# Performance work log

Measured on AMD Instinct MI355X. Metric: run time of the kernel, lower is better.

Reference implementation:

```python
import jax, jax.numpy as jnp
import numpy as np

KS = 3   # window kernel size
NH = 4   # num heads

def unfold3d(x, ks):
    # x: (B,C,D,H,W) -> (B,C,D*H*W, ks**3); matches torch unfold(2).unfold(3).unfold(4) ordering
    B, C, D, H, W = x.shape
    p = ks // 2
    xp = jnp.pad(x, ((0,0),(0,0),(p,p),(p,p),(p,p)))
    wins = [xp[:, :, i:i+D, j:j+H, k:k+W]
            for i in range(ks) for j in range(ks) for k in range(ks)]
    u = jnp.stack(wins, axis=-1)  # (B,C,D,H,W,ks^3)
    return u.reshape(B, C, D*H*W, ks**3)

def make_mask(D, H, W, ks):
    ones = jnp.ones((1, 1, D, H, W), jnp.float32)
    return unfold3d(ones, ks)[0, 0] == 0  # (N, ks^3), True = out-of-bounds (masked)

def l2norm(x, eps=1e-12):
    n = jnp.sqrt(jnp.sum(x * x, axis=-1, keepdims=True))
    return x / jnp.maximum(n, eps)

def layernorm(x, g, b, eps=1e-5):
    m = x.mean(-1, keepdims=True)
    v = x.var(-1, keepdims=True)
    return (x - m) / jnp.sqrt(v + eps) * g + b

def conv3d(x, w, b, pad):
    y = jax.lax.conv_general_dilated(x, w, (1,1,1), [(pad,pad)]*3,
        dimension_numbers=('NCDHW', 'OIDHW', 'NCDHW'))
    return y + b.reshape(1, -1, 1, 1, 1)

def bnorm(x, g, b, eps=1e-5):
    # BatchNorm3d, training-mode batch statistics (biased variance)
    m = x.mean(axis=(0,2,3,4), keepdims=True)
    v = ((x - m) ** 2).mean(axis=(0,2,3,4), keepdims=True)
    return (x - m) / jnp.sqrt(v + eps) * g.reshape(1,-1,1,1,1) + b.reshape(1,-1,1,1,1)

def lrelu(x):
    return jnp.where(x > 0, x, 0.01 * x)

def resblock(x, w1, b1, g1, be1, w2, b2, g2, be2):
    # monai UnetResBlock, in==out, stride 1 -> identity residual
    y = lrelu(bnorm(conv3d(x, w1, b1, 1), g1, be1))
    y = bnorm(conv3d(y, w2, b2, 1), g2, be2)
    return lrelu(y + x)

def epa(x, D, H, W, mask, qkvv_w, temp, temp2, rpb, qemb, op1_w, op1_b, op2_w, op2_b):
    B, N, C = x.shape
    hd = C // NH
    qkvv = (x @ qkvv_w.T).reshape(B, N, 4, NH, hd).transpose(2, 0, 3, 1, 4)  # (4,B,NH,N,hd)
    q, k, v_ca, v_sa = qkvv[0], qkvv[1], qkvv[2], qkvv[3]
    # ---- spatial (local window) attention ----
    qns = (l2norm(q) + qemb) * jax.nn.softplus(temp2)  # (B,NH,N,hd)
    k_flat = k.transpose(0, 1, 3, 2).reshape(B, C, N)
    v_flat = v_sa.transpose(0, 1, 3, 2).reshape(B, C, N)
    k_loc = unfold3d(k_flat.reshape(B, C, D, H, W), KS).reshape(B, NH, hd, N, KS**3).transpose(0, 1, 3, 2, 4)
    v_loc = unfold3d(v_flat.reshape(B, C, D, H, W), KS).reshape(B, NH, hd, N, KS**3).transpose(0, 1, 3, 2, 4)
    attn_sa = jnp.einsum('bhnd,bhndk->bhnk', qns, k_loc) + rpb[None, :, None, :]
    attn_sa = jnp.where(mask[None, None], -jnp.inf, attn_sa)
    attn_sa = jax.nn.softmax(attn_sa, axis=-1)
    # NOTE: original torch code reshapes (B,NH,N,hd) directly to (B,N,C); replicate exactly
    x_sa = jnp.einsum('bhnk,bhndk->bhnd', attn_sa, v_loc).reshape(B, N, C)
    # ---- channel (cosine) cross-attention ----
    qt = l2norm(q.transpose(0, 1, 3, 2))  # (B,NH,hd,N), normalized over N
    kt = l2norm(k.transpose(0, 1, 3, 2))
    attn_ca = jax.nn.softmax(jnp.einsum('bhdn,bhen->bhde', qt, kt) * temp, axis=-1)
    x_ca = jnp.einsum('bhde,bhen->bhdn', attn_ca, v_ca.transpose(0, 1, 3, 2)).transpose(0, 3, 1, 2).reshape(B, N, C)
    return jnp.concatenate([x_sa @ op1_w.T + op1_b, x_ca @ op2_w.T + op2_b], axis=-1)


def setup_inputs() -> dict:
    key = jax.random.key(0)
    B, C, H, W, D = 1, 64, 32, 32, 32
    hd = C // NH
    ks = iter(jax.random.split(key, 40))
    def nrm(shape, s=0.02):
        return jax.random.normal(next(ks), shape, jnp.float32) * s
    inp = {
        'x': jax.random.normal(next(ks), (B, C, H, W, D), jnp.float32),
        'ln_g': jnp.ones((C,), jnp.float32), 'ln_b': jnp.zeros((C,), jnp.float32),
        'gamma': 1e-6 * jnp.ones((C,), jnp.float32),
        'qkvv_w': nrm((4 * C, C)),
        'temp': jnp.ones((NH, 1, 1), jnp.float32), 'temp2': jnp.ones((NH, 1, 1), jnp.float32),
        'rpb': nrm((NH, KS**3), 4e-4),
        'qemb': nrm((NH, 1, hd)),
        'op1_w': nrm((C // 2, C)), 'op1_b': jnp.zeros((C // 2,), jnp.float32),
        'op2_w': nrm((C // 2, C)), 'op2_b': jnp.zeros((C // 2,), jnp.float32),
    }
    for name in ('c51', 'c52'):
        inp[name + '_w1'] = nrm((C, C, 3, 3, 3)); inp[name + '_b1'] = jnp.zeros((C,), jnp.float32)
        inp[name + '_g1'] = jnp.ones((C,), jnp.float32); inp[name + '_be1'] = jnp.zeros((C,), jnp.float32)
        inp[name + '_w2'] = nrm((C, C, 3, 3, 3)); inp[name + '_b2'] = jnp.zeros((C,), jnp.float32)
        inp[name + '_g2'] = jnp.ones((C,), jnp.float32); inp[name + '_be2'] = jnp.zeros((C,), jnp.float32)
    inp['c8_w'] = nrm((C, C, 1, 1, 1)); inp['c8_b'] = jnp.zeros((C,), jnp.float32)
    return inp


def reference(x, ln_g, ln_b, gamma, qkvv_w, temp, temp2, rpb, qemb,
              op1_w, op1_b, op2_w, op2_b,
              c51_w1, c51_b1, c51_g1, c51_be1, c51_w2, c51_b2, c51_g2, c51_be2,
              c52_w1, c52_b1, c52_g1, c52_be1, c52_w2, c52_b2, c52_g2, c52_be2,
              c8_w, c8_b):
    B, C, H, W, D = x.shape
    N = H * W * D
    xs = x.reshape(B, C, N).transpose(0, 2, 1)  # (B,N,C)
    mask = make_mask(D, H, W, KS)
    attn = xs + gamma * epa(layernorm(xs, ln_g, ln_b), D, H, W, mask,
                            qkvv_w, temp, temp2, rpb, qemb, op1_w, op1_b, op2_w, op2_b)
    skip = attn.reshape(B, H, W, D, C).transpose(0, 4, 1, 2, 3)  # (B,C,H,W,D)
    y = resblock(skip, c51_w1, c51_b1, c51_g1, c51_be1, c51_w2, c51_b2, c51_g2, c51_be2)
    y = resblock(y, c52_w1, c52_b1, c52_g1, c52_be1, c52_w2, c52_b2, c52_g2, c52_be2)
    return skip + conv3d(y, c8_w, c8_b, 0)
```

## Files before the change

kernel.cpp:

```cpp
#include <hip/hip_runtime.h>
#include <hip/hip_bf16.h>

typedef __hip_bfloat16 bf16;
typedef __attribute__((ext_vector_type(8))) short s8v;
typedef __attribute__((ext_vector_type(4))) float f4v;

#define NTOT 32768
#define HSZ ((size_t)NTOT*16)

__device__ __forceinline__ float bflo(unsigned int u){ union{unsigned int i;float f;}v; v.i=u<<16; return v.f; }
__device__ __forceinline__ float bfhi(unsigned int u){ union{unsigned int i;float f;}v; v.i=u&0xffff0000u; return v.f; }
__device__ __forceinline__ unsigned short f2bu(float f){ bf16 h = __float2bfloat16(f); unsigned short s; __builtin_memcpy(&s,&h,2); return s; }
__device__ __forceinline__ unsigned int pk2(float a, float b){ return (unsigned int)f2bu(a) | ((unsigned int)f2bu(b)<<16); }

__device__ __forceinline__ void load8(const bf16* p, float* o){
  uint4 u = *(const uint4*)p;
  o[0]=bflo(u.x); o[1]=bfhi(u.x); o[2]=bflo(u.y); o[3]=bfhi(u.y);
  o[4]=bflo(u.z); o[5]=bfhi(u.z); o[6]=bflo(u.w); o[7]=bfhi(u.w);
}
__device__ __forceinline__ void load16(const bf16* p, float* o){
  const uint4* q = (const uint4*)p;
  uint4 u0 = q[0], u1 = q[1];
  o[0]=bflo(u0.x); o[1]=bfhi(u0.x); o[2]=bflo(u0.y); o[3]=bfhi(u0.y);
  o[4]=bflo(u0.z); o[5]=bfhi(u0.z); o[6]=bflo(u0.w); o[7]=bfhi(u0.w);
  o[8]=bflo(u1.x); o[9]=bfhi(u1.x); o[10]=bflo(u1.y); o[11]=bfhi(u1.y);
  o[12]=bflo(u1.z); o[13]=bfhi(u1.z); o[14]=bflo(u1.w); o[15]=bfhi(u1.w);
}
__device__ __forceinline__ void store16(bf16* p, const float* v){
  uint4 u0, u1;
  u0.x=pk2(v[0],v[1]); u0.y=pk2(v[2],v[3]); u0.z=pk2(v[4],v[5]); u0.w=pk2(v[6],v[7]);
  u1.x=pk2(v[8],v[9]); u1.y=pk2(v[10],v[11]); u1.z=pk2(v[12],v[13]); u1.w=pk2(v[14],v[15]);
  uint4* q=(uint4*)p; q[0]=u0; q[1]=u1;
}

__global__ __launch_bounds__(256) void k_qkvv(const float* __restrict__ x,
    const float* __restrict__ lng, const float* __restrict__ lnb,
    const float* __restrict__ w,
    bf16* __restrict__ Qh, bf16* __restrict__ Kh, bf16* __restrict__ Vsh, bf16* __restrict__ Vch)
{
  __shared__ unsigned char sm[64000];
  float* xt = (float*)sm;
  float* mean_s = (float*)(sm + 16896);
  float* rstd_s = (float*)(sm + 16896 + 256);
  float* g_s    = (float*)(sm + 16896 + 512);
  float* b_s    = (float*)(sm + 16896 + 768);
  unsigned char* A2 = sm + 17920;
  unsigned char* Wb = sm + 27136;
  unsigned char* Cout = sm;

  int t = threadIdx.x;
  int n0 = blockIdx.x * 64;
  #pragma unroll
  for (int i=0;i<4;i++){
    int idx = t + i*256; int c = idx>>4, g = idx&15;
    *(float4*)&xt[c*66 + g*4] = *(const float4*)(x + (size_t)c*NTOT + n0 + g*4);
  }
  #pragma unroll
  for (int i=0;i<8;i++){
    int idx = t + i*256; int j = idx>>3, g = idx&7;
    float4 wa = *(const float4*)(w + (size_t)j*64 + g*8);
    float4 wb = *(const float4*)(w + (size_t)j*64 + g*8 + 4);
    uint4 u; u.x=pk2(wa.x,wa.y); u.y=pk2(wa.z,wa.w); u.z=pk2(wb.x,wb.y); u.w=pk2(wb.z,wb.w);
    *(uint4*)(Wb + j*144 + g*16) = u;
  }
  if (t<64){ g_s[t]=lng[t]; b_s[t]=lnb[t]; }
  __syncthreads();
  if (t<64){
    float s=0.f, ss=0.f;
    for (int c=0;c<64;c++){ float v=xt[c*66+t]; s+=v; ss+=v*v; }
    float m = s*(1.f/64.f);
    float var = ss*(1.f/64.f) - m*m;
    mean_s[t]=m; rstd_s[t]=rsqrtf(var+1e-5f);
  }
  __syncthreads();
  {
    int p = t>>2, c0 = (t&3)*16;
    float m = mean_s[p], rs = rstd_s[p];
    unsigned short tmp[16];
    #pragma unroll
    for (int i=0;i<16;i++){
      int c = c0+i;
      tmp[i] = f2bu((xt[c*66+p]-m)*rs*g_s[c] + b_s[c]);
    }
    *(uint4*)(A2 + p*144 + c0*2)      = *(uint4*)&tmp[0];
    *(uint4*)(A2 + p*144 + c0*2 + 16) = *(uint4*)&tmp[8];
  }
  __syncthreads();
  int wv = t>>6, lane = t&63, r = lane&15, q = lane>>4;
  f4v acc[4][4];
  #pragma unroll
  for (int mt=0;mt<4;mt++)
    #pragma unroll
    for (int nt=0;nt<4;nt++){ acc[mt][nt][0]=0.f; acc[mt][nt][1]=0.f; acc[mt][nt][2]=0.f; acc[mt][nt][3]=0.f; }
  #pragma unroll
  for (int ks=0; ks<2; ++ks){
    s8v af[4], bfr[4];
    #pragma unroll
    for (int mt=0;mt<4;mt++) af[mt] = *(const s8v*)(A2 + (mt*16+r)*144 + ks*64 + q*16);
    #pragma unroll
    for (int nt=0;nt<4;nt++) bfr[nt] = *(const s8v*)(Wb + ((wv*4+nt)*16+r)*144 + ks*64 + q*16);
    #pragma unroll
    for (int mt=0;mt<4;mt++)
      #pragma unroll
      for (int nt=0;nt<4;nt++)
        acc[mt][nt] = __builtin_amdgcn_mfma_f32_16x16x32_bf16(af[mt], bfr[nt], acc[mt][nt], 0, 0, 0);
  }
  __syncthreads();
  #pragma unroll
  for (int mt=0;mt<4;mt++)
    #pragma unroll
    for (int nt=0;nt<4;nt++){
      int j = (wv*4+nt)*16 + r;
      #pragma unroll
      for (int reg=0;reg<4;reg++){
        int p = mt*16 + q*4 + reg;
        *(unsigned short*)(Cout + p*528 + j*2) = f2bu(acc[mt][nt][reg]);
      }
    }
  __syncthreads();
  bf16* bases[4] = {Qh, Kh, Vch, Vsh};
  #pragma unroll
  for (int k=0;k<4;k++){
    int chunk = t + k*256;
    int combo = chunk >> 6, pos = chunk & 63;
    int tensor = combo >> 2, h = combo & 3;
    uint4 v = *(const uint4*)(Cout + pos*528 + (tensor*64 + h*16)*2);
    *(uint4*)((unsigned char*)bases[tensor] + ((size_t)h*HSZ + (size_t)(n0+pos)*16)*2) = v;
  }
}

__global__ __launch_bounds__(256) void k_chanpart(const bf16* __restrict__ Qh, const bf16* __restrict__ Kh,
    float* __restrict__ G, float* __restrict__ NQ, float* __restrict__ NK)
{
  int h = blockIdx.y;
  int t = threadIdx.x; int d = t>>4, e = t&15;
  __shared__ float qs[128][16];
  __shared__ float ks[128][16];
  float acc=0.f, accq=0.f, acck=0.f;
  for (int stage=0; stage<2; ++stage){
    int n0 = blockIdx.x*256 + stage*128;
    __syncthreads();
    {
      int row = t & 127, which = t >> 7;
      const bf16* p = (which ? Kh : Qh) + ((size_t)h*NTOT + n0 + row)*16;
      float tmp[16]; load16(p, tmp);
      float* dst = which ? &ks[row][0] : &qs[row][0];
      #pragma unroll
      for (int i=0;i<16;i++) dst[i]=tmp[i];
    }
    __syncthreads();
    for (int i=0;i<128;i++){
      float qv = qs[i][d], kv = ks[i][e];
      acc += qv*kv;
      if (e==0) accq += qv*qv;
      if (e==1){ float kd = ks[i][d]; acck += kd*kd; }
    }
  }
  atomicAdd(&G[(h*16+d)*16+e], acc);
  if (e==0) atomicAdd(&NQ[h*16+d], accq);
  if (e==1) atomicAdd(&NK[h*16+d], acck);
}

__global__ __launch_bounds__(256) void k_spatial(const bf16* __restrict__ Qh, const bf16* __restrict__ Kh,
    const bf16* __restrict__ Vsh, const bf16* __restrict__ Vch,
    const float* __restrict__ G, const float* __restrict__ NQ, const float* __restrict__ NK,
    const float* __restrict__ temp, const float* __restrict__ temp2,
    const float* __restrict__ rpb, const float* __restrict__ qemb,
    bf16* __restrict__ xsa, bf16* __restrict__ xca)
{
  __shared__ float aca_s[1024];
  __shared__ float rpb_s[108];
  __shared__ float qemb_s[64];
  int t = threadIdx.x;
  if (t < 64){
    int hh = t>>4;
    float tp = temp[hh];
    float nq = fmaxf(sqrtf(NQ[t]), 1e-12f);
    float sv[16]; float mx=-3.0e38f;
    #pragma unroll
    for (int e=0;e<16;e++){
      float nk = fmaxf(sqrtf(NK[hh*16+e]), 1e-12f);
      sv[e] = G[t*16+e] / (nq*nk) * tp;
      mx = fmaxf(mx, sv[e]);
    }
    float sum=0.f;
    #pragma unroll
    for (int e=0;e<16;e++){ sv[e]=expf(sv[e]-mx); sum+=sv[e]; }
    float inv = 1.f/sum;
    #pragma unroll
    for (int e=0;e<16;e++) aca_s[t*16+e] = sv[e]*inv;
  }
  if (t<108) rpb_s[t]=rpb[t];
  if (t<64) qemb_s[t]=qemb[t];
  __syncthreads();
  int lane = t & 63, h = t >> 6;
  int n = blockIdx.x*64 + lane;
  int a = n>>10, b=(n>>5)&31, c=n&31;
  const bf16* Kb = Kh + (size_t)h*HSZ;
  const bf16* Vb = Vsh + (size_t)h*HSZ;
  float q[16]; load16(Qh + (size_t)h*HSZ + (size_t)n*16, q);
  float s2=0.f;
  #pragma unroll
  for (int d=0;d<16;d++) s2 += q[d]*q[d];
  float inv = 1.f/fmaxf(sqrtf(s2), 1e-12f);
  float st2 = log1pf(expf(temp2[h]));
  #pragma unroll
  for (int d=0;d<16;d++) q[d] = (q[d]*inv + qemb_s[h*16+d])*st2;
  float sc[27]; float mx = -3.0e38f;
  #pragma unroll
  for (int kk=0;kk<27;kk++){
    int da=kk/9-1, db=(kk/3)%3-1, dc=kk%3-1;
    int aa=a+da, bb=b+db, cc=c+dc;
    float s = -3.0e38f;
    if ((unsigned)aa<32u && (unsigned)bb<32u && (unsigned)cc<32u){
      int nn = n + da*1024 + db*32 + dc;
      float kv[16]; load16(Kb + (size_t)nn*16, kv);
      s = rpb_s[h*27+kk];
      #pragma unroll
      for (int d=0;d<16;d++) s += q[d]*kv[d];
    }
    sc[kk]=s; mx = fmaxf(mx, s);
  }
  float sum=0.f;
  #pragma unroll
  for (int kk=0;kk<27;kk++){ float e = expf(sc[kk]-mx); sc[kk]=e; sum+=e; }
  float invs = 1.f/sum;
  float o[16];
  #pragma unroll
  for (int d=0;d<16;d++) o[d]=0.f;
  #pragma unroll
  for (int kk=0;kk<27;kk++){
    int da=kk/9-1, db=(kk/3)%3-1, dc=kk%3-1;
    int aa=a+da, bb=b+db, cc=c+dc;
    if ((unsigned)aa<32u && (unsigned)bb<32u && (unsigned)cc<32u){
      int nn = n + da*1024 + db*32 + dc;
      float vv[16]; load16(Vb + (size_t)nn*16, vv);
      float p = sc[kk];
      #pragma unroll
      for (int d=0;d<16;d++) o[d] += p*vv[d];
    }
  }
  #pragma unroll
  for (int d=0;d<16;d++) o[d]*=invs;
  store16(xsa + ((size_t)h*NTOT + n)*16, o);
  float vca[16]; load16(Vch + (size_t)h*HSZ + (size_t)n*16, vca);
  float oc[16];
  #pragma unroll
  for (int d=0;d<16;d++){
    float s=0.f;
    #pragma unroll
    for (int e=0;e<16;e++) s += aca_s[(h*16+d)*16+e]*vca[e];
    oc[d]=s;
  }
  store16(xca + (size_t)n*64 + h*16, oc);
}

__global__ __launch_bounds__(256) void k_epilogue(const float* __restrict__ x,
    const bf16* __restrict__ xsa, const bf16* __restrict__ xca,
    const float* __restrict__ op1w, const float* __restrict__ op1b,
    const float* __restrict__ op2w, const float* __restrict__ op2b,
    const float* __restrict__ gamma, float* __restrict__ skipf)
{
  __shared__ float xs_s[64][68];
  __shared__ float xc_s[64][68];
  __shared__ float trans[64][68];
  int t = threadIdx.x;
  int n0 = blockIdx.x * 64;
  #pragma unroll
  for (int it=0; it<2; ++it){
    int idx = t + it*256;
    int p = idx >> 3, cg = idx & 7;
    float a8[8], c8[8];
    load8(xsa + (size_t)(n0+p)*64 + cg*8, a8);
    load8(xca + (size_t)(n0+p)*64 + cg*8, c8);
    #pragma unroll
    for (int i=0;i<8;i++){ xs_s[p][cg*8+i]=a8[i]; xc_s[p][cg*8+i]=c8[i]; }
  }
  int co = t & 63, pg = t >> 6;
  const float* wrow = (co < 32) ? (op1w + (size_t)co*64) : (op2w + (size_t)(co-32)*64);
  float wreg[64];
  #pragma unroll
  for (int i=0;i<16;i++) *(float4*)&wreg[i*4] = *(const float4*)(wrow + i*4);
  float bv = (co<32) ? op1b[co] : op2b[co-32];
  float gv = gamma[co];
  __syncthreads();
  const float* xt = (co<32) ? &xs_s[0][0] : &xc_s[0][0];
  float out16[16];
  #pragma unroll
  for (int i=0;i<16;i++){
    int p = pg*16 + i;
    const float* xr = xt + p*68;
    float s = bv;
    #pragma unroll
    for (int k4=0;k4<16;k4++){
      float4 xv = *(const float4*)(xr + k4*4);
      s += wreg[k4*4]*xv.x + wreg[k4*4+1]*xv.y + wreg[k4*4+2]*xv.z + wreg[k4*4+3]*xv.w;
    }
    out16[i] = s;
  }
  size_t base = (size_t)co*NTOT + n0 + pg*16;
  #pragma unroll
  for (int i4=0;i4<4;i4++){
    float4 xv = *(const float4*)(x + base + i4*4);
    out16[i4*4]   = xv.x + gv*out16[i4*4];
    out16[i4*4+1] = xv.y + gv*out16[i4*4+1];
    out16[i4*4+2] = xv.z + gv*out16[i4*4+2];
    out16[i4*4+3] = xv.w + gv*out16[i4*4+3];
  }
  #pragma unroll
  for (int i=0;i<16;i++) trans[pg*16+i][co] = out16[i];
  __syncthreads();
  {
    int pos = t >> 2, grp = t & 3;
    float* dst = skipf + (size_t)(n0+pos)*64 + grp*16;
    #pragma unroll
    for (int i4=0;i4<4;i4++)
      *(float4*)(dst + i4*4) = *(const float4*)&trans[pos][grp*16 + i4*4];
  }
}

__global__ void k_wprep(const float* __restrict__ wA, const float* __restrict__ wB_,
    const float* __restrict__ wC, const float* __restrict__ wD,
    const float* __restrict__ w8, bf16* __restrict__ WB, float* __restrict__ w8t)
{
  int idx = blockIdx.x*256 + threadIdx.x;
  if (idx < 458752){
    int j = idx & 7;
    int rr = (idx>>3) & 15;
    int q = (idx>>7) & 3;
    int nt = (idx>>9) & 3;
    int rest = idx >> 11;
    int tp = rest % 14;
    int rest2 = rest / 14;
    int cc = rest2 & 3;
    int conv = rest2 >> 2;
    int co = nt*16 + rr;
    int tap = 2*tp + (q>>1);
    int ci = cc*16 + (q&1)*8 + j;
    const float* src = conv==0?wA:conv==1?wB_:conv==2?wC:wD;
    float v = (tap < 27) ? src[((size_t)co*64 + ci)*27 + tap] : 0.f;
    WB[idx] = __float2bfloat16(v);
  }
  if (idx < 4096){ int ci = idx>>6, co = idx&63; w8t[ci*64+co] = w8[(size_t)co*64+ci]; }
}

template<int MODE>
__global__ __launch_bounds__(256, 2) void k_conv3x(const void* __restrict__ src,
    const float* __restrict__ stats, const float* __restrict__ g, const float* __restrict__ be,
    const float* __restrict__ resid,
    const bf16* __restrict__ WB, const float* __restrict__ bias,
    bf16* __restrict__ Yout, float* __restrict__ BNpart)
{
  __shared__ float smf[17408];
  unsigned char* smb = (unsigned char*)smf;
  int t = threadIdx.x;
  int w = t >> 6, lane = t & 63;
  int r = lane & 15, q = lane >> 4;
  int qe = q & 1, qh = q >> 1;
  int a = blockIdx.x >> 4, b0 = (blockIdx.x & 15) * 2;
  int hh = t & 7;

  float m8[8], rs8[8], be8[8];
  if (MODE != 0){
    #pragma unroll
    for (int i=0;i<8;i++){
      int ci = hh*8 + i;
      float S = stats[ci*2], SS = stats[ci*2+1];
      float m = S*(1.f/NTOT);
      m8[i] = m;
      rs8[i] = rsqrtf(SS*(1.f/NTOT) - m*m + 1e-5f) * g[ci];
      be8[i] = be[ci];
    }
  }

  if (MODE == 0){
    #pragma unroll
    for (int c0=0;c0<2;++c0){
      int kb = c0*7, kn = (c0==0)?7:6;
      float4 f0[7], f1[7]; int fl[7];
      #pragma unroll
      for (int k=0;k<7;k++){
        fl[k]=0;
        if (k<kn){
          int idx = t + (kb+k)*256;
          if (idx < 3264){
            int pos = idx>>3;
            int par=pos/136, rem=pos-par*136, pbr=rem/34, pc=rem-pbr*34;
            int pa=a+par, pb=b0+pbr;
            fl[k]=1;
            if (pa>=1&&pa<=32&&pb>=1&&pb<=32&&pc>=1&&pc<=32){
              int nsrc=(pa-1)*1024+(pb-1)*32+(pc-1);
              const float* p = (const float*)src + (size_t)nsrc*64 + hh*8;
              f0[k]=*(const float4*)p; f1[k]=*(const float4*)(p+4);
              fl[k]=2;
            }
          }
        }
      }
      #pragma unroll
      for (int k=0;k<7;k++){
        if (k<kn && fl[k]){
          int pos = (t + (kb+k)*256)>>3;
          uint4 o={0,0,0,0};
          if (fl[k]==2){
            o.x=pk2(f0[k].x,f0[k].y); o.y=pk2(f0[k].z,f0[k].w);
            o.z=pk2(f1[k].x,f1[k].y); o.w=pk2(f1[k].z,f1[k].w);
          }
          *(uint4*)(smb + pos*144 + hh*16) = o;
        }
      }
    }
  } else {
    const int CS = (MODE==2)?5:13;
    const int NC = (MODE==2)?3:1;
    #pragma unroll
    for (int c0=0;c0<NC;++c0){
      int kb = c0*CS;
      int kn = (MODE==2) ? ((c0==2)?3:5) : 13;
      uint4 u[CS]; float4 r0[CS], r1[CS]; int fl[CS];
      #pragma unroll
      for (int k=0;k<CS;k++){
        fl[k]=0;
        if (k<kn){
          int idx = t + (kb+k)*256;
          if (idx < 3264){
            int pos = idx>>3;
            int par=pos/136, rem=pos-par*136, pbr=rem/34, pc=rem-pbr*34;
            int pa=a+par, pb=b0+pbr;
            fl[k]=1;
            if (pa>=1&&pa<=32&&pb>=1&&pb<=32&&pc>=1&&pc<=32){
              int nsrc=(pa-1)*1024+(pb-1)*32+(pc-1);
              u[k] = *(const uint4*)((const unsigned char*)src + ((size_t)nsrc*64 + hh*8)*2);
              if (MODE==2){
                const float* rp = resid + (size_t)nsrc*64 + hh*8;
                r0[k]=*(const float4*)rp; r1[k]=*(const float4*)(rp+4);
              }
              fl[k]=2;
            }
          }
        }
      }
      #pragma unroll
      for (int k=0;k<CS;k++){
        if (k<kn && fl[k]){
          int pos = (t + (kb+k)*256)>>3;
          uint4 o={0,0,0,0};
          if (fl[k]==2){
            float v[8];
            v[0]=bflo(u[k].x); v[1]=bfhi(u[k].x); v[2]=bflo(u[k].y); v[3]=bfhi(u[k].y);
            v[4]=bflo(u[k].z); v[5]=bfhi(u[k].z); v[6]=bflo(u[k].w); v[7]=bfhi(u[k].w);
            float rv[8];
            if (MODE==2){
              rv[0]=r0[k].x; rv[1]=r0[k].y; rv[2]=r0[k].z; rv[3]=r0[k].w;
              rv[4]=r1[k].x; rv[5]=r1[k].y; rv[6]=r1[k].z; rv[7]=r1[k].w;
            }
            #pragma unroll
            for (int i=0;i<8;i++){
              float y = (v[i]-m8[i])*rs8[i] + be8[i];
              if (MODE==2) y += rv[i];
              v[i] = y>0.f ? y : 0.01f*y;
            }
            o.x=pk2(v[0],v[1]); o.y=pk2(v[2],v[3]); o.z=pk2(v[4],v[5]); o.w=pk2(v[6],v[7]);
          }
          *(uint4*)(smb + pos*144 + hh*16) = o;
        }
      }
    }
  }

  int toff[14];
  #pragma unroll
  for (int tp=0;tp<14;++tp){
    int tap = 2*tp + qh;
    int da = tap/9, rem = tap - da*9, db = rem/3, dc = rem - db*3;
    toff[tp] = (tap<27) ? (((da*4+db)*34 + dc)*144) : 0;
  }
  int F[4];
  #pragma unroll
  for (int mt=0;mt<4;mt++) F[mt] = (((mt>>1)*34 + (mt&1)*16 + r)*144) + w*32 + qe*16;
  const unsigned char* wbp = (const unsigned char*)WB + (size_t)w*57344 + lane*16;

  f4v acc[4][4];
  #pragma unroll
  for (int mt=0;mt<4;mt++)
    #pragma unroll
    for (int nt=0;nt<4;nt++){ acc[mt][nt][0]=0.f; acc[mt][nt][1]=0.f; acc[mt][nt][2]=0.f; acc[mt][nt][3]=0.f; }

  __syncthreads();

  s8v aC[4], bC[4], bN[4];
  #pragma unroll
  for (int mt=0;mt<4;mt++) aC[mt] = *(const s8v*)(smb + F[mt] + toff[0]);
  #pragma unroll
  for (int nt=0;nt<4;nt++){ bC[nt] = *(const s8v*)(wbp + nt*1024); bN[nt] = *(const s8v*)(wbp + 4096 + nt*1024); }

  #pragma unroll
  for (int tp=0; tp<14; ++tp){
    s8v aN[4], bN2[4];
    if (tp < 12){
      #pragma unroll
      for (int nt=0;nt<4;nt++) bN2[nt] = *(const s8v*)(wbp + (tp+2)*4096 + nt*1024);
    }
    if (tp < 13){
      #pragma unroll
      for (int mt=0;mt<4;mt++) aN[mt] = *(const s8v*)(smb + F[mt] + toff[tp+1]);
    }
    #pragma unroll
    for (int mt=0;mt<4;mt++)
      #pragma unroll
      for (int nt=0;nt<4;nt++)
        acc[mt][nt] = __builtin_amdgcn_mfma_f32_16x16x32_bf16(aC[mt], bC[nt], acc[mt][nt], 0, 0, 0);
    #pragma unroll
    for (int nt=0;nt<4;nt++) bC[nt] = bN[nt];
    if (tp < 12){
      #pragma unroll
      for (int nt=0;nt<4;nt++) bN[nt] = bN2[nt];
    }
    if (tp < 13){
      #pragma unroll
      for (int mt=0;mt<4;mt++) aC[mt] = aN[mt];
    }
  }

  __syncthreads();
  #pragma unroll
  for (int mt=0;mt<4;mt++)
    #pragma unroll
    for (int nt=0;nt<4;nt++)
      *(float4*)&smf[w*4352 + (nt*16+r)*68 + mt*16 + q*4] = *(float4*)&acc[mt][nt];
  __syncthreads();

  float vals[16];
  {
    int co = t >> 2, pg = t & 3;
    float bv = bias[co];
    #pragma unroll
    for (int i4=0;i4<4;i4++){
      int p = pg*16 + i4*4;
      float4 s0 = *(const float4*)&smf[0*4352 + co*68 + p];
      float4 s1 = *(const float4*)&smf[1*4352 + co*68 + p];
      float4 s2 = *(const float4*)&smf[2*4352 + co*68 + p];
      float4 s3 = *(const float4*)&smf[3*4352 + co*68 + p];
      vals[i4*4+0] = s0.x+s1.x+s2.x+s3.x+bv;
      vals[i4*4+1] = s0.y+s1.y+s2.y+s3.y+bv;
      vals[i4*4+2] = s0.z+s1.z+s2.z+s3.z+bv;
      vals[i4*4+3] = s0.w+s1.w+s2.w+s3.w+bv;
    }
    float s=0.f, ss=0.f;
    #pragma unroll
    for (int i=0;i<16;i++){ s+=vals[i]; ss+=vals[i]*vals[i]; }
    s += __shfl_xor(s,1); ss += __shfl_xor(ss,1);
    s += __shfl_xor(s,2); ss += __shfl_xor(ss,2);
    if (pg==0){
      BNpart[(size_t)blockIdx.x*128 + co*2]     = s;
      BNpart[(size_t)blockIdx.x*128 + co*2 + 1] = ss;
    }
  }
  __syncthreads();
  {
    int co = t >> 2, pg = t & 3;
    #pragma unroll
    for (int i=0;i<16;i++) smf[(pg*16+i)*68 + co] = vals[i];
  }
  __syncthreads();
  {
    int pos = t >> 2, grp = t & 3;
    float v16[16];
    #pragma unroll
    for (int i4=0;i4<4;i4++) *(float4*)&v16[i4*4] = *(const float4*)&smf[pos*68 + grp*16 + i4*4];
    uint4 u0, u1;
    u0.x=pk2(v16[0],v16[1]); u0.y=pk2(v16[2],v16[3]); u0.z=pk2(v16[4],v16[5]); u0.w=pk2(v16[6],v16[7]);
    u1.x=pk2(v16[8],v16[9]); u1.y=pk2(v16[10],v16[11]); u1.z=pk2(v16[12],v16[13]); u1.w=pk2(v16[14],v16[15]);
    int nb = a*1024 + (b0 + (pos>>5))*32 + (pos&31);
    uint4* dst = (uint4*)((unsigned char*)Yout + ((size_t)nb*64 + grp*16)*2);
    dst[0] = u0; dst[1] = u1;
  }
}

__global__ __launch_bounds__(1024) void k_bnred(const float* __restrict__ BNpart, float* __restrict__ BNout)
{
  __shared__ float red[8][128];
  int t = threadIdx.x;
  int col = t & 127, grp = t >> 7;
  float acc = 0.f;
  #pragma unroll 8
  for (int r = grp*64; r < grp*64 + 64; ++r) acc += BNpart[r*128 + col];
  red[grp][col] = acc;
  __syncthreads();
  if (grp == 0){
    float s = 0.f;
    #pragma unroll
    for (int g=0; g<8; g++) s += red[g][col];
    BNout[col] = s;
  }
}

__global__ __launch_bounds__(256) void k_conv1f(const bf16* __restrict__ Y4,
    const float* __restrict__ BN4, const float* __restrict__ g4, const float* __restrict__ be4,
    const bf16* __restrict__ Y2, const float* __restrict__ BN2,
    const float* __restrict__ g2, const float* __restrict__ be2,
    const float* __restrict__ skipf, const float* __restrict__ w8t, const float* __restrict__ b8,
    float* __restrict__ out)
{
  __shared__ float R2[64][68];
  __shared__ float skT[64][68];
  __shared__ float wt[4096];
  __shared__ float bs[64];
  int t = threadIdx.x;
  int n0 = blockIdx.x * 64;
  #pragma unroll
  for (int k=0;k<4;k++){
    int idx = t + k*256;
    *(float4*)&wt[idx*4] = *(const float4*)(w8t + idx*4);
  }
  if (t < 64) bs[t] = b8[t];
  {
    int pos = t >> 2, grp = t & 3;
    int n = n0 + pos;
    float y2[16], y4[16], sk[16];
    load16(Y2 + (size_t)n*64 + grp*16, y2);
    load16(Y4 + (size_t)n*64 + grp*16, y4);
    #pragma unroll
    for (int i4=0;i4<4;i4++) *(float4*)&sk[i4*4] = *(const float4*)(skipf + (size_t)n*64 + grp*16 + i4*4);
    #pragma unroll
    for (int i=0;i<16;i++){
      int ci = grp*16+i;
      float S2=BN2[ci*2], SS2=BN2[ci*2+1];
      float m2=S2*(1.f/NTOT);
      float r2v=rsqrtf(SS2*(1.f/NTOT)-m2*m2+1e-5f);
      float R = (y2[i]-m2)*r2v*g2[ci]+be2[ci] + sk[i];
      R = R>0.f ? R : 0.01f*R;
      float S4=BN4[ci*2], SS4=BN4[ci*2+1];
      float m4=S4*(1.f/NTOT);
      float r4v=rsqrtf(SS4*(1.f/NTOT)-m4*m4+1e-5f);
      float vy = (y4[i]-m4)*r4v*g4[ci]+be4[ci] + R;
      vy = vy>0.f ? vy : 0.01f*vy;
      R2[ci][pos] = vy;
      skT[ci][pos] = sk[i];
    }
  }
  __syncthreads();
  int lane = t & 63, cg = t >> 6;
  float acc[16];
  #pragma unroll
  for (int j=0;j<16;j++) acc[j]=0.f;
  for (int ci=0; ci<64; ci++){
    float rv = R2[ci][lane];
    const float* wr = &wt[ci*64 + cg*16];
    float4 wa = *(const float4*)(wr);
    float4 wb = *(const float4*)(wr+4);
    float4 wc = *(const float4*)(wr+8);
    float4 wd = *(const float4*)(wr+12);
    acc[0]+=rv*wa.x; acc[1]+=rv*wa.y; acc[2]+=rv*wa.z; acc[3]+=rv*wa.w;
    acc[4]+=rv*wb.x; acc[5]+=rv*wb.y; acc[6]+=rv*wb.z; acc[7]+=rv*wb.w;
    acc[8]+=rv*wc.x; acc[9]+=rv*wc.y; acc[10]+=rv*wc.z; acc[11]+=rv*wc.w;
    acc[12]+=rv*wd.x; acc[13]+=rv*wd.y; acc[14]+=rv*wd.z; acc[15]+=rv*wd.w;
  }
  #pragma unroll
  for (int j=0;j<16;j++){
    int co = cg*16+j;
    out[(size_t)co*NTOT + n0 + lane] = acc[j] + bs[co] + skT[co][lane];
  }
}

extern "C" void kernel_launch(void* const* d_in, const int* in_sizes, int n_in,
                              void* d_out, int out_size, void* d_ws, size_t ws_size,
                              hipStream_t stream) {
  (void)in_sizes; (void)n_in; (void)out_size; (void)ws_size;
  const float* x      = (const float*)d_in[0];
  const float* ln_g   = (const float*)d_in[1];
  const float* ln_b   = (const float*)d_in[2];
  const float* gamma  = (const float*)d_in[3];
  const float* qkvv_w = (const float*)d_in[4];
  const float* temp   = (const float*)d_in[5];
  const float* temp2  = (const float*)d_in[6];
  const float* rpb    = (const float*)d_in[7];
  const float* qemb   = (const float*)d_in[8];
  const float* op1w   = (const float*)d_in[9];
  const float* op1b   = (const float*)d_in[10];
  const float* op2w   = (const float*)d_in[11];
  const float* op2b   = (const float*)d_in[12];
  const float* c51_w1 = (const float*)d_in[13];
  const float* c51_b1 = (const float*)d_in[14];
  const float* c51_g1 = (const float*)d_in[15];
  const float* c51_be1= (const float*)d_in[16];
  const float* c51_w2 = (const float*)d_in[17];
  const float* c51_b2 = (const float*)d_in[18];
  const float* c51_g2 = (const float*)d_in[19];
  const float* c51_be2= (const float*)d_in[20];
  const float* c52_w1 = (const float*)d_in[21];
  const float* c52_b1 = (const float*)d_in[22];
  const float* c52_g1 = (const float*)d_in[23];
  const float* c52_be1= (const float*)d_in[24];
  const float* c52_w2 = (const float*)d_in[25];
  const float* c52_b2 = (const float*)d_in[26];
  const float* c52_g2 = (const float*)d_in[27];
  const float* c52_be2= (const float*)d_in[28];
  const float* c8_w   = (const float*)d_in[29];
  const float* c8_b   = (const float*)d_in[30];

  unsigned char* ws = (unsigned char*)d_ws;
  const size_t MB = 1u<<20;
  bf16*  Qh   = (bf16*)(ws + 0);
  bf16*  Kh   = (bf16*)(ws + 4*MB);
  bf16*  Vsh  = (bf16*)(ws + 8*MB);
  bf16*  Vch  = (bf16*)(ws + 12*MB);
  bf16*  xsa  = (bf16*)(ws + 16*MB);
  bf16*  xca  = (bf16*)(ws + 20*MB);
  float* skipf= (float*)(ws + 24*MB);
  float* stat = (float*)(ws + 32*MB);
  float* G    = stat + 0;
  float* NQ   = stat + 1024;
  float* NK   = stat + 1088;
  float* BN1  = stat + 1152;
  float* BN2  = stat + 1312;
  float* BN3  = stat + 1472;
  float* BN4  = stat + 1632;
  bf16*  WB   = (bf16*)(ws + 33*MB);
  float* w8t  = (float*)(ws + 33*MB + 1048576);
  float* BNpart = (float*)(ws + 35*MB);
  bf16*  Y1   = (bf16*)(ws + 36*MB);
  bf16*  Y2   = (bf16*)(ws + 40*MB);
  bf16*  Y3   = (bf16*)(ws + 44*MB);
  bf16*  Y4   = (bf16*)(ws + 48*MB);

  hipMemsetAsync(stat, 0, 1152*sizeof(float), stream);
  k_wprep<<<1792,256,0,stream>>>(c51_w1, c51_w2, c52_w1, c52_w2, c8_w, WB, w8t);
  k_qkvv<<<512,256,0,stream>>>(x, ln_g, ln_b, qkvv_w, Qh, Kh, Vsh, Vch);
  k_chanpart<<<dim3(128,4),256,0,stream>>>(Qh, Kh, G, NQ, NK);
  k_spatial<<<512,256,0,stream>>>(Qh, Kh, Vsh, Vch, G, NQ, NK, temp, temp2, rpb, qemb, xsa, xca);
  k_epilogue<<<512,256,0,stream>>>(x, xsa, xca, op1w, op1b, op2w, op2b, gamma, skipf);
  k_conv3x<0><<<512,256,0,stream>>>(skipf, nullptr, nullptr, nullptr, nullptr, WB + 0*114688, c51_b1, Y1, BNpart);
  k_bnred<<<1,1024,0,stream>>>(BNpart, BN1);
  k_conv3x<1><<<512,256,0,stream>>>(Y1, BN1, c51_g1, c51_be1, nullptr, WB + 1*114688, c51_b2, Y2, BNpart);
  k_bnred<<<1,1024,0,stream>>>(BNpart, BN2);
  k_conv3x<2><<<512,256,0,stream>>>(Y2, BN2, c51_g2, c51_be2, skipf, WB + 2*114688, c52_b1, Y3, BNpart);
  k_bnred<<<1,1024,0,stream>>>(BNpart, BN3);
  k_conv3x<1><<<512,256,0,stream>>>(Y3, BN3, c52_g1, c52_be1, nullptr, WB + 3*114688, c52_b2, Y4, BNpart);
  k_bnred<<<1,1024,0,stream>>>(BNpart, BN4);
  k_conv1f<<<512,256,0,stream>>>(Y4, BN4, c52_g2, c52_be2, Y2, BN2, c51_g2, c51_be2, skipf, w8t, c8_b, (float*)d_out);
}
```

Baseline: 288.4 us.

## Fuse BN partial reduction into conv kernels via last-block atomic counter

Removes the four separate single-block k_bnred launches. Each conv3x block now bumps an atomic counter after writing its partials, and the last block to finish reduces them into the BN statistics. The stats memset is folded into k_wprep, and k_chanpart processes twice as many rows per block with half the grid. The trade is fewer launches and less serialization against a threadfence, an atomic, and a final reduction that runs on a single block; BN4 is moved to avoid overlapping the counters.

```diff
diff --git a/kernel.cpp b/kernel.cpp
--- a/kernel.cpp
+++ b/kernel.cpp
@@ -137,8 +137,8 @@
   __shared__ float qs[128][16];
   __shared__ float ks[128][16];
   float acc=0.f, accq=0.f, acck=0.f;
-  for (int stage=0; stage<2; ++stage){
-    int n0 = blockIdx.x*256 + stage*128;
+  for (int stage=0; stage<4; ++stage){
+    int n0 = blockIdx.x*512 + stage*128;
     __syncthreads();
     {
       int row = t & 127, which = t >> 7;
@@ -321,9 +321,12 @@
 
 __global__ void k_wprep(const float* __restrict__ wA, const float* __restrict__ wB_,
     const float* __restrict__ wC, const float* __restrict__ wD,
-    const float* __restrict__ w8, bf16* __restrict__ WB, float* __restrict__ w8t)
+    const float* __restrict__ w8, bf16* __restrict__ WB, float* __restrict__ w8t,
+    float* __restrict__ statz)
 {
   int idx = blockIdx.x*256 + threadIdx.x;
+  if (idx < 1152) statz[idx] = 0.f;
+  if (idx >= 1664 && idx < 1668) statz[idx] = 0.f;
   if (idx < 458752){
     int j = idx & 7;
     int rr = (idx>>3) & 15;
@@ -349,7 +352,8 @@
     const float* __restrict__ stats, const float* __restrict__ g, const float* __restrict__ be,
     const float* __restrict__ resid,
     const bf16* __restrict__ WB, const float* __restrict__ bias,
-    bf16* __restrict__ Yout, float* __restrict__ BNpart)
+    bf16* __restrict__ Yout, float* __restrict__ BNpart,
+    float* __restrict__ BNout, unsigned int* __restrict__ ctr)
 {
   __shared__ float smf[17408];
   unsigned char* smb = (unsigned char*)smf;
@@ -575,23 +579,20 @@
     uint4* dst = (uint4*)((unsigned char*)Yout + ((size_t)nb*64 + grp*16)*2);
     dst[0] = u0; dst[1] = u1;
   }
-}
-
-__global__ __launch_bounds__(1024) void k_bnred(const float* __restrict__ BNpart, float* __restrict__ BNout)
-{
-  __shared__ float red[8][128];
-  int t = threadIdx.x;
-  int col = t & 127, grp = t >> 7;
-  float acc = 0.f;
-  #pragma unroll 8
-  for (int r = grp*64; r < grp*64 + 64; ++r) acc += BNpart[r*128 + col];
-  red[grp][col] = acc;
-  __syncthreads();
-  if (grp == 0){
-    float s = 0.f;
-    #pragma unroll
-    for (int g=0; g<8; g++) s += red[g][col];
-    BNout[col] = s;
+  __threadfence();
+  __syncthreads();
+  unsigned int* flag = (unsigned int*)smf;
+  if (t == 0) flag[0] = (atomicAdd(ctr, 1u) == 511u) ? 1u : 0u;
+  __syncthreads();
+  if (flag[0]){
+    int col = t & 127, half = t >> 7;
+    float acc2 = 0.f;
+    #pragma unroll 8
+    for (int rr2 = half*256; rr2 < half*256+256; ++rr2) acc2 += BNpart[rr2*128 + col];
+    float* red = smf + 64;
+    red[half*128 + col] = acc2;
+    __syncthreads();
+    if (t < 128) BNout[t] = red[t] + red[128 + t];
   }
 }
 
@@ -716,6 +717,7 @@
   float* BN2  = stat + 1312;
   float* BN3  = stat + 1472;
   float* BN4  = stat + 1632;
+  unsigned int* ctrs = (unsigned int*)(stat + 1664);
   bf16*  WB   = (bf16*)(ws + 33*MB);
   float* w8t  = (float*)(ws + 33*MB + 1048576);
   float* BNpart = (float*)(ws + 35*MB);
@@ -724,19 +726,16 @@
   bf16*  Y3   = (bf16*)(ws + 44*MB);
   bf16*  Y4   = (bf16*)(ws + 48*MB);
 
-  hipMemsetAsync(stat, 0, 1152*sizeof(float), stream);
-  k_wprep<<<1792,256,0,stream>>>(c51_w1, c51_w2, c52_w1, c52_w2, c8_w, WB, w8t);
+  BN4 = stat + 1792;
+
+  k_wprep<<<1792,256,0,stream>>>(c51_w1, c51_w2, c52_w1, c52_w2, c8_w, WB, w8t, stat);
   k_qkvv<<<512,256,0,stream>>>(x, ln_g, ln_b, qkvv_w, Qh, Kh, Vsh, Vch);
-  k_chanpart<<<dim3(128,4),256,0,stream>>>(Qh, Kh, G, NQ, NK);
+  k_chanpart<<<dim3(64,4),256,0,stream>>>(Qh, Kh, G, NQ, NK);
   k_spatial<<<512,256,0,stream>>>(Qh, Kh, Vsh, Vch, G, NQ, NK, temp, temp2, rpb, qemb, xsa, xca);
   k_epilogue<<<512,256,0,stream>>>(x, xsa, xca, op1w, op1b, op2w, op2b, gamma, skipf);
-  k_conv3x<0><<<512,256,0,stream>>>(skipf, nullptr, nullptr, nullptr, nullptr, WB + 0*114688, c51_b1, Y1, BNpart);
-  k_bnred<<<1,1024,0,stream>>>(BNpart, BN1);
-  k_conv3x<1><<<512,256,0,stream>>>(Y1, BN1, c51_g1, c51_be1, nullptr, WB + 1*114688, c51_b2, Y2, BNpart);
-  k_bnred<<<1,1024,0,stream>>>(BNpart, BN2);
-  k_conv3x<2><<<512,256,0,stream>>>(Y2, BN2, c51_g2, c51_be2, skipf, WB + 2*114688, c52_b1, Y3, BNpart);
-  k_bnred<<<1,1024,0,stream>>>(BNpart, BN3);
-  k_conv3x<1><<<512,256,0,stream>>>(Y3, BN3, c52_g1, c52_be1, nullptr, WB + 3*114688, c52_b2, Y4, BNpart);
-  k_bnred<<<1,1024,0,stream>>>(BNpart, BN4);
+  k_conv3x<0><<<512,256,0,stream>>>(skipf, nullptr, nullptr, nullptr, nullptr, WB + 0*114688, c51_b1, Y1, BNpart, BN1, ctrs+0);
+  k_conv3x<1><<<512,256,0,stream>>>(Y1, BN1, c51_g1, c51_be1, nullptr, WB + 1*114688, c51_b2, Y2, BNpart, BN2, ctrs+1);
+  k_conv3x<2><<<512,256,0,stream>>>(Y2, BN2, c51_g2, c51_be2, skipf, WB + 2*114688, c52_b1, Y3, BNpart, BN3, ctrs+2);
+  k_conv3x<1><<<512,256,0,stream>>>(Y3, BN3, c52_g1, c52_be1, nullptr, WB + 3*114688, c52_b2, Y4, BNpart, BN4, ctrs+3);
   k_conv1f<<<512,256,0,stream>>>(Y4, BN4, c52_g2, c52_be2, Y2, BN2, c51_g2, c51_be2, skipf, w8t, c8_b, (float*)d_out);
 }
```

Result: slower. 524.1 us (+81.7%).

## Fuse attention epilogue projections into spatial kernel and fold memset into wprep

Applied to the files above, without the earlier changes.

Merges the output-projection epilogue into the spatial attention kernel, so the bf16 xsa/xca intermediates no longer go to global memory and one launch is removed. The spatial output is staged in shared memory using the reshaped head layout, and the final skip rows are written with a scattered index mapping instead of a transposed coalesced store. The stats memset moves into the weight-prep kernel, and chanpart now runs on half as many blocks, each covering twice as many rows. The scattered per-element skipf stores and strided x reads may be less coalesced than before.

```diff
diff --git a/kernel.cpp b/kernel.cpp
--- a/kernel.cpp
+++ b/kernel.cpp
@@ -13,11 +13,6 @@
 __device__ __forceinline__ unsigned short f2bu(float f){ bf16 h = __float2bfloat16(f); unsigned short s; __builtin_memcpy(&s,&h,2); return s; }
 __device__ __forceinline__ unsigned int pk2(float a, float b){ return (unsigned int)f2bu(a) | ((unsigned int)f2bu(b)<<16); }
 
-__device__ __forceinline__ void load8(const bf16* p, float* o){
-  uint4 u = *(const uint4*)p;
-  o[0]=bflo(u.x); o[1]=bfhi(u.x); o[2]=bflo(u.y); o[3]=bfhi(u.y);
-  o[4]=bflo(u.z); o[5]=bfhi(u.z); o[6]=bflo(u.w); o[7]=bfhi(u.w);
-}
 __device__ __forceinline__ void load16(const bf16* p, float* o){
   const uint4* q = (const uint4*)p;
   uint4 u0 = q[0], u1 = q[1];
@@ -25,12 +20,6 @@
   o[4]=bflo(u0.z); o[5]=bfhi(u0.z); o[6]=bflo(u0.w); o[7]=bfhi(u0.w);
   o[8]=bflo(u1.x); o[9]=bfhi(u1.x); o[10]=bflo(u1.y); o[11]=bfhi(u1.y);
   o[12]=bflo(u1.z); o[13]=bfhi(u1.z); o[14]=bflo(u1.w); o[15]=bfhi(u1.w);
-}
-__device__ __forceinline__ void store16(bf16* p, const float* v){
-  uint4 u0, u1;
-  u0.x=pk2(v[0],v[1]); u0.y=pk2(v[2],v[3]); u0.z=pk2(v[4],v[5]); u0.w=pk2(v[6],v[7]);
-  u1.x=pk2(v[8],v[9]); u1.y=pk2(v[10],v[11]); u1.z=pk2(v[12],v[13]); u1.w=pk2(v[14],v[15]);
-  uint4* q=(uint4*)p; q[0]=u0; q[1]=u1;
 }
 
 __global__ __launch_bounds__(256) void k_qkvv(const float* __restrict__ x,
@@ -137,8 +126,8 @@
   __shared__ float qs[128][16];
   __shared__ float ks[128][16];
   float acc=0.f, accq=0.f, acck=0.f;
-  for (int stage=0; stage<2; ++stage){
-    int n0 = blockIdx.x*256 + stage*128;
+  for (int stage=0; stage<4; ++stage){
+    int n0 = blockIdx.x*512 + stage*128;
     __syncthreads();
     {
       int row = t & 127, which = t >> 7;
@@ -166,12 +155,18 @@
     const float* __restrict__ G, const float* __restrict__ NQ, const float* __restrict__ NK,
     const float* __restrict__ temp, const float* __restrict__ temp2,
     const float* __restrict__ rpb, const float* __restrict__ qemb,
-    bf16* __restrict__ xsa, bf16* __restrict__ xca)
+    const float* __restrict__ x,
+    const float* __restrict__ op1w, const float* __restrict__ op1b,
+    const float* __restrict__ op2w, const float* __restrict__ op2b,
+    const float* __restrict__ gamma, float* __restrict__ skipf)
 {
   __shared__ float aca_s[1024];
   __shared__ float rpb_s[108];
   __shared__ float qemb_s[64];
+  __shared__ float xs_s[64][68];
+  __shared__ float xc_s[64][68];
   int t = threadIdx.x;
+  int n0 = blockIdx.x * 64;
   if (t < 64){
     int hh = t>>4;
     float tp = temp[hh];
@@ -194,7 +189,7 @@
   if (t<64) qemb_s[t]=qemb[t];
   __syncthreads();
   int lane = t & 63, h = t >> 6;
-  int n = blockIdx.x*64 + lane;
+  int n = n0 + lane;
   int a = n>>10, b=(n>>5)&31, c=n&31;
   const bf16* Kb = Kh + (size_t)h*HSZ;
   const bf16* Vb = Vsh + (size_t)h*HSZ;
@@ -240,42 +235,22 @@
       for (int d=0;d<16;d++) o[d] += p*vv[d];
     }
   }
-  #pragma unroll
-  for (int d=0;d<16;d++) o[d]*=invs;
-  store16(xsa + ((size_t)h*NTOT + n)*16, o);
-  float vca[16]; load16(Vch + (size_t)h*HSZ + (size_t)n*16, vca);
-  float oc[16];
-  #pragma unroll
-  for (int d=0;d<16;d++){
-    float s=0.f;
-    #pragma unroll
-    for (int e=0;e<16;e++) s += aca_s[(h*16+d)*16+e]*vca[e];
-    oc[d]=s;
-  }
-  store16(xca + (size_t)n*64 + h*16, oc);
-}
-
-__global__ __launch_bounds__(256) void k_epilogue(const float* __restrict__ x,
-    const bf16* __restrict__ xsa, const bf16* __restrict__ xca,
-    const float* __restrict__ op1w, const float* __restrict__ op1b,
-    const float* __restrict__ op2w, const float* __restrict__ op2b,
-    const float* __restrict__ gamma, float* __restrict__ skipf)
-{
-  __shared__ float xs_s[64][68];
-  __shared__ float xc_s[64][68];
-  __shared__ float trans[64][68];
-  int t = threadIdx.x;
-  int n0 = blockIdx.x * 64;
-  #pragma unroll
-  for (int it=0; it<2; ++it){
-    int idx = t + it*256;
-    int p = idx >> 3, cg = idx & 7;
-    float a8[8], c8[8];
-    load8(xsa + (size_t)(n0+p)*64 + cg*8, a8);
-    load8(xca + (size_t)(n0+p)*64 + cg*8, c8);
-    #pragma unroll
-    for (int i=0;i<8;i++){ xs_s[p][cg*8+i]=a8[i]; xc_s[p][cg*8+i]=c8[i]; }
-  }
+  {
+    int jrow = h*16 + (lane>>2), cbase = (lane&3)*16;
+    #pragma unroll
+    for (int d=0;d<16;d++) xs_s[jrow][cbase + d] = o[d]*invs;
+  }
+  {
+    float vca[16]; load16(Vch + (size_t)h*HSZ + (size_t)n*16, vca);
+    #pragma unroll
+    for (int d=0;d<16;d++){
+      float s=0.f;
+      #pragma unroll
+      for (int e=0;e<16;e++) s += aca_s[(h*16+d)*16+e]*vca[e];
+      xc_s[lane][h*16+d] = s;
+    }
+  }
+  __syncthreads();
   int co = t & 63, pg = t >> 6;
   const float* wrow = (co < 32) ? (op1w + (size_t)co*64) : (op2w + (size_t)(co-32)*64);
   float wreg[64];
@@ -283,47 +258,31 @@
   for (int i=0;i<16;i++) *(float4*)&wreg[i*4] = *(const float4*)(wrow + i*4);
   float bv = (co<32) ? op1b[co] : op2b[co-32];
   float gv = gamma[co];
-  __syncthreads();
-  const float* xt = (co<32) ? &xs_s[0][0] : &xc_s[0][0];
-  float out16[16];
+  const float* xt_ = (co<32) ? &xs_s[0][0] : &xc_s[0][0];
   #pragma unroll
   for (int i=0;i<16;i++){
     int p = pg*16 + i;
-    const float* xr = xt + p*68;
+    const float* xr = xt_ + p*68;
     float s = bv;
     #pragma unroll
     for (int k4=0;k4<16;k4++){
       float4 xv = *(const float4*)(xr + k4*4);
       s += wreg[k4*4]*xv.x + wreg[k4*4+1]*xv.y + wreg[k4*4+2]*xv.z + wreg[k4*4+3]*xv.w;
     }
-    out16[i] = s;
-  }
-  size_t base = (size_t)co*NTOT + n0 + pg*16;
-  #pragma unroll
-  for (int i4=0;i4<4;i4++){
-    float4 xv = *(const float4*)(x + base + i4*4);
-    out16[i4*4]   = xv.x + gv*out16[i4*4];
-    out16[i4*4+1] = xv.y + gv*out16[i4*4+1];
-    out16[i4*4+2] = xv.z + gv*out16[i4*4+2];
-    out16[i4*4+3] = xv.w + gv*out16[i4*4+3];
-  }
-  #pragma unroll
-  for (int i=0;i<16;i++) trans[pg*16+i][co] = out16[i];
-  __syncthreads();
-  {
-    int pos = t >> 2, grp = t & 3;
-    float* dst = skipf + (size_t)(n0+pos)*64 + grp*16;
-    #pragma unroll
-    for (int i4=0;i4<4;i4++)
-      *(float4*)(dst + i4*4) = *(const float4*)&trans[pos][grp*16 + i4*4];
+    int m;
+    if (co < 32){ int hh2 = p>>4, jj = p&15; m = hh2*8192 + (n0>>2) + jj; }
+    else m = n0 + p;
+    skipf[(size_t)m*64 + co] = x[(size_t)co*NTOT + m] + gv*s;
   }
 }
 
 __global__ void k_wprep(const float* __restrict__ wA, const float* __restrict__ wB_,
     const float* __restrict__ wC, const float* __restrict__ wD,
-    const float* __restrict__ w8, bf16* __restrict__ WB, float* __restrict__ w8t)
+    const float* __restrict__ w8, bf16* __restrict__ WB, float* __restrict__ w8t,
+    float* __restrict__ statz)
 {
   int idx = blockIdx.x*256 + threadIdx.x;
+  if (idx < 1152) statz[idx] = 0.f;
   if (idx < 458752){
     int j = idx & 7;
     int rr = (idx>>3) & 15;
@@ -705,8 +664,6 @@
   bf16*  Kh   = (bf16*)(ws + 4*MB);
   bf16*  Vsh  = (bf16*)(ws + 8*MB);
   bf16*  Vch  = (bf16*)(ws + 12*MB);
-  bf16*  xsa  = (bf16*)(ws + 16*MB);
-  bf16*  xca  = (bf16*)(ws + 20*MB);
   float* skipf= (float*)(ws + 24*MB);
   float* stat = (float*)(ws + 32*MB);
   float* G    = stat + 0;
@@ -724,12 +681,11 @@
   bf16*  Y3   = (bf16*)(ws + 44*MB);
   bf16*  Y4   = (bf16*)(ws + 48*MB);
 
-  hipMemsetAsync(stat, 0, 1152*sizeof(float), stream);
-  k_wprep<<<1792,256,0,stream>>>(c51_w1, c51_w2, c52_w1, c52_w2, c8_w, WB, w8t);
+  k_wprep<<<1792,256,0,stream>>>(c51_w1, c51_w2, c52_w1, c52_w2, c8_w, WB, w8t, stat);
   k_qkvv<<<512,256,0,stream>>>(x, ln_g, ln_b, qkvv_w, Qh, Kh, Vsh, Vch);
-  k_chanpart<<<dim3(128,4),256,0,stream>>>(Qh, Kh, G, NQ, NK);
-  k_spatial<<<512,256,0,stream>>>(Qh, Kh, Vsh, Vch, G, NQ, NK, temp, temp2, rpb, qemb, xsa, xca);
-  k_epilogue<<<512,256,0,stream>>>(x, xsa, xca, op1w, op1b, op2w, op2b, gamma, skipf);
+  k_chanpart<<<dim3(64,4),256,0,stream>>>(Qh, Kh, G, NQ, NK);
+  k_spatial<<<512,256,0,stream>>>(Qh, Kh, Vsh, Vch, G, NQ, NK, temp, temp2, rpb, qemb,
+                                  x, op1w, op1b, op2w, op2b, gamma, skipf);
   k_conv3x<0><<<512,256,0,stream>>>(skipf, nullptr, nullptr, nullptr, nullptr, WB + 0*114688, c51_b1, Y1, BNpart);
   k_bnred<<<1,1024,0,stream>>>(BNpart, BN1);
   k_conv3x<1><<<512,256,0,stream>>>(Y1, BN1, c51_g1, c51_be1, nullptr, WB + 1*114688, c51_b2, Y2, BNpart);
```

After: 288.3 us (median of 2 runs). Within noise of the previous version (-0.0%).
